# Kernel optimization log

Hardware: AMD Instinct MI355X
Metric: run time of the kernel (lower is better)

Reference implementation:

```python
import jax, jax.numpy as jnp
import numpy as np

N, E, P, D, G, L = 100000, 640000, 640000, 128, 128, 3
BN_EPS = 1e-5

def _bn(x, p):
    # eval-mode BatchNorm1d: p is stacked [gamma, beta, running_mean, running_var]
    g, b, m, v = p[0], p[1], p[2], p[3]
    return (x - m) * jax.lax.rsqrt(v + BN_EPS) * g + b

def setup_inputs() -> dict:
    key = jax.random.key(0)
    ks = iter(jax.random.split(key, 64))
    def nrm(shape, s):
        return jax.random.normal(next(ks), shape, jnp.float32) * s
    def bnp(shape):
        return jax.random.uniform(next(ks), shape, jnp.float32, 0.5, 1.5)
    inp = {}
    # graph data
    inp['x_node'] = jnp.zeros((N,), jnp.int32)
    inp['edge_index'] = jax.random.randint(next(ks), (2, E), 0, N, jnp.int32)
    inp['edge_attr'] = jax.random.normal(next(ks), (E, 7), jnp.float32)
    inp['batch'] = jnp.sort(jax.random.randint(next(ks), (N,), 0, G, jnp.int32))
    inp['pos_index'] = jax.random.randint(next(ks), (P,), 0, 1800, jnp.int32)
    inp['pos_enc'] = jax.random.uniform(next(ks), (P,), jnp.float32)
    inp['pos_batch'] = jnp.sort(jax.random.randint(next(ks), (P,), 0, E, jnp.int32))
    # encoders
    inp['node_emb'] = nrm((1, D), 1.0)                 # Embedding(1, D) for ogbg-ppa
    inp['z_init'] = nrm((1800, D), 1.0)                # z_initial embedding table
    inp['ze_bn1'] = bnp((4, D))
    inp['ze_W'] = nrm((D, D), D ** -0.5)
    inp['ze_b'] = jnp.zeros((D,), jnp.float32)
    inp['ze_bn2'] = bnp((4, D))
    inp['vn_emb'] = jnp.zeros((1, D), jnp.float32)     # init.constant_(0)
    # GINConv_eff per-layer params (stacked over L)
    inp['conv_We'] = nrm((L, 7, D), 7 ** -0.5)         # edge_encoder Linear(7, D)
    inp['conv_be'] = jnp.zeros((L, D), jnp.float32)
    inp['conv_Wp'] = nrm((L, D, D), D ** -0.5)         # edge_encoder_pos Linear(D, D)
    inp['conv_bp'] = jnp.zeros((L, D), jnp.float32)
    inp['conv_W1'] = nrm((L, D, 2 * D), D ** -0.5)     # mlp Linear(D, 2D)
    inp['conv_b1'] = jnp.zeros((L, 2 * D), jnp.float32)
    inp['conv_bn'] = bnp((L, 4, 2 * D))                # mlp BatchNorm(2D)
    inp['conv_W2'] = nrm((L, 2 * D, D), (2 * D) ** -0.5)  # mlp Linear(2D, D)
    inp['conv_b2'] = jnp.zeros((L, D), jnp.float32)
    inp['conv_eps'] = jnp.zeros((L,), jnp.float32)     # GIN eps, init 0
    inp['layer_bn'] = bnp((L, 4, D))                   # per-layer batch_norms
    # virtual-node MLPs (L-1 of them)
    inp['vn_W1'] = nrm((L - 1, D, 2 * D), D ** -0.5)
    inp['vn_b1'] = jnp.zeros((L - 1, 2 * D), jnp.float32)
    inp['vn_bn1'] = bnp((L - 1, 4, 2 * D))
    inp['vn_W2'] = nrm((L - 1, 2 * D, D), (2 * D) ** -0.5)
    inp['vn_b2'] = jnp.zeros((L - 1, D), jnp.float32)
    inp['vn_bn2'] = bnp((L - 1, 4, D))
    return inp

def reference(x_node, edge_index, edge_attr, batch, pos_index, pos_enc, pos_batch,
              node_emb, z_init, ze_bn1, ze_W, ze_b, ze_bn2, vn_emb,
              conv_We, conv_be, conv_Wp, conv_bp, conv_W1, conv_b1, conv_bn,
              conv_W2, conv_b2, conv_eps, layer_bn,
              vn_W1, vn_b1, vn_bn1, vn_W2, vn_b2, vn_bn2):
    src, dst = edge_index[0], edge_index[1]
    # node encoder (Embedding(1, D) indexed by zeros)
    h = node_emb[x_node]                                           # [N, D]
    # positional edge embedding: pool z_initial rows per edge, then z_embedding MLP
    z = jax.ops.segment_sum(z_init[pos_index] * pos_enc[:, None], pos_batch,
                            num_segments=E)                        # [E, D]
    z = jax.nn.relu(_bn(z, ze_bn1))
    z = jax.nn.relu(_bn(z @ ze_W + ze_b, ze_bn2))
    # virtual node embeddings, one per graph
    vn = jnp.broadcast_to(vn_emb[0], (G, D))
    for l in range(L):
        h_in = h + vn[batch]                                       # virtual-node broadcast add
        # GINConv_eff
        edge_emb = edge_attr @ conv_We[l] + conv_be[l] + z @ conv_Wp[l] + conv_bp[l]  # [E, D]
        msg = jax.nn.relu(h_in[src] + edge_emb)                    # gather + relu
        agg = jax.ops.segment_sum(msg, dst, num_segments=N)        # scatter-add
        t = (1.0 + conv_eps[l]) * h_in + agg
        t = jax.nn.relu(_bn(t @ conv_W1[l] + conv_b1[l], conv_bn[l]))
        out = t @ conv_W2[l] + conv_b2[l]
        out = _bn(out, layer_bn[l])                                # batch_norms[l]
        h = out if l == L - 1 else jax.nn.relu(out)                # dropout is identity (eval)
        if l < L - 1:
            vt = jax.ops.segment_sum(h_in, batch, num_segments=G) + vn
            vt = jax.nn.relu(_bn(vt @ vn_W1[l] + vn_b1[l], vn_bn1[l]))
            vn = jax.nn.relu(_bn(vt @ vn_W2[l] + vn_b2[l], vn_bn2[l]))
    return h  # JK == 'last'
```

## Files before the change

kernel.cpp:

```cpp
#include <hip/hip_runtime.h>
#include <hip/hip_bf16.h>

typedef __hip_bfloat16 bf16;
typedef __attribute__((ext_vector_type(8))) short short8;
typedef __attribute__((ext_vector_type(4))) float floatx4;

constexpr int Nn = 100000;
constexpr int Ee = 640000;
constexpr int Pp = 640000;
constexpr int Gg = 128;
constexpr int Ll = 3;
#define Dd 128
#define BN_EPS 1e-5f

__device__ __forceinline__ float b2f(bf16 x) { return __bfloat162float(x); }
__device__ __forceinline__ bf16 f2b(float x) { return __float2bfloat16(x); }
#define MFMA16 __builtin_amdgcn_mfma_f32_16x16x32_bf16

union U8 { uint4 u; bf16 h[8]; short8 s; };

__global__ void k_estart(const int* __restrict__ pos_batch, int* __restrict__ estart) {
  int e = blockIdx.x * blockDim.x + threadIdx.x;
  if (e > Ee) return;
  int lo = 0, hi = Pp;
  while (lo < hi) { int mid = (lo + hi) >> 1; if (pos_batch[mid] < e) lo = mid + 1; else hi = mid; }
  estart[e] = lo;
}

__global__ void k_hist(const int* __restrict__ dst, int* __restrict__ cnt) {
  int e = blockIdx.x * blockDim.x + threadIdx.x;
  if (e >= Ee) return;
  atomicAdd(&cnt[dst[e]], 1);
}

__global__ void k_scanA(const int* __restrict__ cnt, int* __restrict__ rs,
                        int* __restrict__ chunkSum) {
  __shared__ int buf[1024];
  int tid = threadIdx.x;
  int i = blockIdx.x * 1024 + tid;
  int v = (i < Nn) ? cnt[i] : 0;
  buf[tid] = v;
  __syncthreads();
  for (int off = 1; off < 1024; off <<= 1) {
    int t = (tid >= off) ? buf[tid - off] : 0;
    __syncthreads();
    buf[tid] += t;
    __syncthreads();
  }
  if (i < Nn) rs[i] = buf[tid] - v;
  if (tid == 1023) chunkSum[blockIdx.x] = buf[1023];
}

__global__ void k_scanC(int* __restrict__ rs, const int* __restrict__ chunkSum) {
  __shared__ int offS;
  if (threadIdx.x == 0) {
    int o = 0;
    for (int j = 0; j < blockIdx.x; ++j) o += chunkSum[j];
    offS = o;
  }
  __syncthreads();
  int i = blockIdx.x * 1024 + threadIdx.x;
  if (i < Nn) rs[i] += offS;
}

__global__ void k_scatter(const int* __restrict__ dst, const int* __restrict__ rs,
                          int* __restrict__ cur, int* __restrict__ perm) {
  int e = blockIdx.x * blockDim.x + threadIdx.x;
  if (e >= Ee) return;
  int d = dst[e];
  int r = atomicAdd(&cur[d], 1);
  perm[rs[d] + r] = e;
}

__global__ void k_permcopy(const int* __restrict__ perm, const int* __restrict__ src,
                           const int* __restrict__ dst, const int* __restrict__ estart,
                           const float* __restrict__ eattr,
                           int* __restrict__ src_p, int* __restrict__ dst_p,
                           int2* __restrict__ rng_p, bf16* __restrict__ ea_p) {
  int i = blockIdx.x * blockDim.x + threadIdx.x;
  if (i >= Ee) return;
  int e = perm[i];
  src_p[i] = src[e];
  dst_p[i] = dst[e];
  rng_p[i] = make_int2(estart[e], estart[e + 1]);
  U8 o;
  #pragma unroll
  for (int j = 0; j < 7; ++j) o.h[j] = f2b(eattr[(size_t)e * 7 + j]);
  o.h[7] = f2b(1.0f);
  ((uint4*)ea_p)[i] = o.u;
}

__global__ void k_prep(const float* __restrict__ zeW, const float* __restrict__ Wp,
                       const float* __restrict__ We, const float* __restrict__ be,
                       const float* __restrict__ bp,
                       const float* __restrict__ W1, const float* __restrict__ W2,
                       bf16* __restrict__ zeWsw, bf16* __restrict__ WpSw,
                       bf16* __restrict__ WeSw, bf16* __restrict__ W1sw,
                       bf16* __restrict__ W2sw) {
  int gid = blockIdx.x * blockDim.x + threadIdx.x;
  if (gid < 16384) {
    int i = gid;
    int j = i & 7, lane = (i >> 3) & 63, t = (i >> 9) & 7, kc = i >> 12;
    int k = kc * 32 + ((lane >> 4) * 8) + j, n = t * 16 + (lane & 15);
    zeWsw[i] = f2b(zeW[k * 128 + n]);
  }
  if (gid < 49152) {
    int l = gid / 16384, i = gid % 16384;
    int j = i & 7, lane = (i >> 3) & 63, t = (i >> 9) & 7, kc = i >> 12;
    int k = kc * 32 + ((lane >> 4) * 8) + j, n = t * 16 + (lane & 15);
    WpSw[gid] = f2b(Wp[l * 16384 + k * 128 + n]);
  }
  if (gid < 12288) {
    int l = gid / 4096, i = gid % 4096;
    int j = i & 7, lane = (i >> 3) & 63, t = i >> 9;
    int k = ((lane >> 4) * 8) + j, n = t * 16 + (lane & 15);
    float v = 0.f;
    if (k < 7) v = We[l * 896 + k * 128 + n];
    else if (k == 7) v = be[l * 128 + n] + bp[l * 128 + n];
    WeSw[gid] = f2b(v);
  }
  if (gid < 98304) {
    int l = gid / 32768, i = gid % 32768;
    int j = i & 7, lane = (i >> 3) & 63, t = (i >> 9) & 15, kc = i >> 13;
    int k = kc * 32 + ((lane >> 4) * 8) + j, n = t * 16 + (lane & 15);
    W1sw[gid] = f2b(W1[l * 32768 + k * 256 + n]);
  }
  if (gid < 98304) {
    int l = gid / 32768, i = gid % 32768;
    int j = i & 7, lane = (i >> 3) & 63, t = (i >> 9) & 7, kc = i >> 12;
    int k = kc * 32 + ((lane >> 4) * 8) + j, n = t * 16 + (lane & 15);
    W2sw[gid] = f2b(W2[l * 32768 + k * 128 + n]);
  }
}

__global__ void k_bnfold(const float* __restrict__ ze_bn1, const float* __restrict__ ze_b,
                         const float* __restrict__ ze_bn2,
                         const float* __restrict__ conv_b1, const float* __restrict__ conv_bn,
                         const float* __restrict__ conv_b2, const float* __restrict__ layer_bn,
                         const float* __restrict__ vn_b1, const float* __restrict__ vn_bn1,
                         const float* __restrict__ vn_b2, const float* __restrict__ vn_bn2,
                         float* __restrict__ fb) {
  int i = blockIdx.x * blockDim.x + threadIdx.x;
  if (i < 128) {
    float g = ze_bn1[i], b = ze_bn1[128 + i], m = ze_bn1[256 + i], v = ze_bn1[384 + i];
    float s = g * rsqrtf(v + BN_EPS);
    fb[i] = s; fb[128 + i] = b - m * s;
  } else if (i < 256) {
    int c = i - 128;
    float g = ze_bn2[c], b = ze_bn2[128 + c], m = ze_bn2[256 + c], v = ze_bn2[384 + c];
    float s = g * rsqrtf(v + BN_EPS);
    fb[256 + c] = s; fb[384 + c] = b - m * s + s * ze_b[c];
  } else if (i < 1024) {
    int j = i - 256; int l = j >> 8, c = j & 255;
    const float* bn = conv_bn + (size_t)l * 1024;
    float g = bn[c], b = bn[256 + c], m = bn[512 + c], v = bn[768 + c];
    float s = g * rsqrtf(v + BN_EPS);
    fb[512 + j] = s; fb[1280 + j] = b - m * s + s * conv_b1[l * 256 + c];
  } else if (i < 1408) {
    int j = i - 1024; int l = j >> 7, c = j & 127;
    const float* bn = layer_bn + (size_t)l * 512;
    float g = bn[c], b = bn[128 + c], m = bn[256 + c], v = bn[384 + c];
    float s = g * rsqrtf(v + BN_EPS);
    fb[2048 + j] = s; fb[2432 + j] = b - m * s + s * conv_b2[l * 128 + c];
  } else if (i < 1920) {
    int j = i - 1408; int l = j >> 8, c = j & 255;
    const float* bn = vn_bn1 + (size_t)l * 1024;
    float g = bn[c], b = bn[256 + c], m = bn[512 + c], v = bn[768 + c];
    float s = g * rsqrtf(v + BN_EPS);
    fb[2816 + j] = s; fb[3328 + j] = b - m * s + s * vn_b1[l * 256 + c];
  } else if (i < 2176) {
    int j = i - 1920; int l = j >> 7, c = j & 127;
    const float* bn = vn_bn2 + (size_t)l * 512;
    float g = bn[c], b = bn[128 + c], m = bn[256 + c], v = bn[384 + c];
    float s = g * rsqrtf(v + BN_EPS);
    fb[3840 + j] = s; fb[4096 + j] = b - m * s + s * vn_b2[l * 128 + c];
  }
}

__global__ void k_init_vn(const float* __restrict__ vn_emb, float* __restrict__ vn) {
  int gid = blockIdx.x * blockDim.x + threadIdx.x;
  if (gid >= Gg * 128) return;
  vn[gid] = vn_emb[gid & 127];
}

__global__ void k_hin0(const int* __restrict__ x_node, const float* __restrict__ node_emb,
                       const float* __restrict__ vn, const int* __restrict__ batch,
                       bf16* __restrict__ h_in) {
  int gid = blockIdx.x * blockDim.x + threadIdx.x;
  if (gid >= Nn * 16) return;
  int n = gid >> 4, c = gid & 15;
  int x = x_node[n], b = batch[n];
  float4 a0 = ((const float4*)node_emb)[x * 32 + c * 2];
  float4 a1 = ((const float4*)node_emb)[x * 32 + c * 2 + 1];
  float4 v0 = ((const float4*)vn)[b * 32 + c * 2];
  float4 v1 = ((const float4*)vn)[b * 32 + c * 2 + 1];
  U8 o;
  o.h[0] = f2b(a0.x + v0.x); o.h[1] = f2b(a0.y + v0.y);
  o.h[2] = f2b(a0.z + v0.z); o.h[3] = f2b(a0.w + v0.w);
  o.h[4] = f2b(a1.x + v1.x); o.h[5] = f2b(a1.y + v1.y);
  o.h[6] = f2b(a1.z + v1.z); o.h[7] = f2b(a1.w + v1.w);
  ((uint4*)h_in)[gid] = o.u;
}

__global__ __launch_bounds__(256, 4) void k_edge_z(
    const int2* __restrict__ rng_perm, const int* __restrict__ pos_index,
    const float* __restrict__ pos_enc, const float* __restrict__ z_init,
    const float* __restrict__ fb, const bf16* __restrict__ zeWsw,
    const bf16* __restrict__ ea_p, const int* __restrict__ src_p,
    const int* __restrict__ dst_p, const bf16* __restrict__ h_in,
    const bf16* __restrict__ WpSw, const bf16* __restrict__ WeSw,
    bf16* __restrict__ Z, int store_z, float* agg) {
  __shared__ bf16 Az[64][136];
  __shared__ int dstS[64];
  int tid = threadIdx.x;
  int lane = tid & 63, wv = tid >> 6;
  int q = lane >> 4, ln = lane & 15;
  int e0 = blockIdx.x * 64;

  if (q == 0) dstS[16 * wv + ln] = dst_p[e0 + 16 * wv + ln];
  short8 af0 = {};
  if (q == 0) af0 = *(const short8*)(ea_p + (size_t)(e0 + 16 * wv + ln) * 8);

  {
    int r = lane >> 2, cc = lane & 3;
    int2 rg = rng_perm[e0 + 16 * wv + r];
    float acc[32];
    #pragma unroll
    for (int j = 0; j < 32; ++j) acc[j] = 0.f;
    for (int p = rg.x; p < rg.y; ++p) {
      int idx = pos_index[p];
      float w = pos_enc[p];
      #pragma unroll
      for (int qq = 0; qq < 8; ++qq) {
        float4 z4 = ((const float4*)z_init)[idx * 32 + cc * 8 + qq];
        acc[qq * 4 + 0] = fmaf(w, z4.x, acc[qq * 4 + 0]);
        acc[qq * 4 + 1] = fmaf(w, z4.y, acc[qq * 4 + 1]);
        acc[qq * 4 + 2] = fmaf(w, z4.z, acc[qq * 4 + 2]);
        acc[qq * 4 + 3] = fmaf(w, z4.w, acc[qq * 4 + 3]);
      }
    }
    #pragma unroll
    for (int qq = 0; qq < 4; ++qq) {
      U8 o;
      #pragma unroll
      for (int jj = 0; jj < 2; ++jj) {
        int col = cc * 32 + qq * 8 + jj * 4;
        float4 s4 = *(const float4*)&fb[col];
        float4 h4 = *(const float4*)&fb[128 + col];
        o.h[jj * 4 + 0] = f2b(fmaxf(0.f, fmaf(acc[qq * 8 + jj * 4 + 0], s4.x, h4.x)));
        o.h[jj * 4 + 1] = f2b(fmaxf(0.f, fmaf(acc[qq * 8 + jj * 4 + 1], s4.y, h4.y)));
        o.h[jj * 4 + 2] = f2b(fmaxf(0.f, fmaf(acc[qq * 8 + jj * 4 + 2], s4.z, h4.z)));
        o.h[jj * 4 + 3] = f2b(fmaxf(0.f, fmaf(acc[qq * 8 + jj * 4 + 3], s4.w, h4.w)));
      }
      *(uint4*)&Az[16 * wv + r][cc * 32 + qq * 8] = o.u;
    }
  }
  __builtin_amdgcn_wave_barrier();

  {
    floatx4 acc1[8] = {};
    #pragma unroll
    for (int kc = 0; kc < 4; ++kc) {
      short8 af = *(const short8*)&Az[16 * wv + ln][kc * 32 + q * 8];
      #pragma unroll
      for (int t = 0; t < 8; ++t) {
        short8 bfr = *(const short8*)(zeWsw + (((size_t)kc * 8 + t) * 64 + lane) * 8);
        acc1[t] = MFMA16(af, bfr, acc1[t], 0, 0, 0);
      }
    }
    __builtin_amdgcn_wave_barrier();
    #pragma unroll
    for (int t = 0; t < 8; ++t) {
      int c = t * 16 + ln;
      float ss = fb[256 + c], hh = fb[384 + c];
      #pragma unroll
      for (int r = 0; r < 4; ++r)
        Az[16 * wv + q * 4 + r][c] = f2b(fmaxf(0.f, fmaf(acc1[t][r], ss, hh)));
    }
  }
  __builtin_amdgcn_wave_barrier();
  floatx4 acc2[8] = {};
  #pragma unroll
  for (int t = 0; t < 8; ++t) {
    short8 bfr = *(const short8*)(WeSw + ((size_t)t * 64 + lane) * 8);
    acc2[t] = MFMA16(af0, bfr, acc2[t], 0, 0, 0);
  }
  #pragma unroll
  for (int kc = 0; kc < 4; ++kc) {
    short8 af = *(const short8*)&Az[16 * wv + ln][kc * 32 + q * 8];
    #pragma unroll
    for (int t = 0; t < 8; ++t) {
      short8 bfr = *(const short8*)(WpSw + (((size_t)kc * 8 + t) * 64 + lane) * 8);
      acc2[t] = MFMA16(af, bfr, acc2[t], 0, 0, 0);
    }
  }
  __builtin_amdgcn_wave_barrier();
  if (store_z) {
    #pragma unroll
    for (int p = 0; p < 4; ++p) {
      int row = 16 * wv + p * 4 + q;
      uint4 vv = *(const uint4*)&Az[row][ln * 8];
      ((uint4*)Z)[(size_t)(e0 + row) * 16 + ln] = vv;
    }
  }
  __builtin_amdgcn_wave_barrier();
  #pragma unroll
  for (int p = 0; p < 4; ++p) {
    int el = 16 * wv + p * 4 + q;
    int s = src_p[e0 + el];
    uint4 hh = ((const uint4*)h_in)[(size_t)s * 16 + ln];
    *(uint4*)&Az[el][ln * 8] = hh;
  }
  __builtin_amdgcn_wave_barrier();
  #pragma unroll
  for (int t = 0; t < 8; ++t) {
    int c = t * 16 + ln;
    #pragma unroll
    for (int r = 0; r < 4; ++r) {
      int el = 16 * wv + q * 4 + r;
      Az[el][c] = f2b(fmaxf(0.f, acc2[t][r] + b2f(Az[el][c])));
    }
  }
  __builtin_amdgcn_wave_barrier();
  {
    float s0 = 0.f, s1 = 0.f;
    int dprev = dstS[16 * wv];
    bool inside = false;
    #pragma unroll
    for (int j = 0; j < 16; ++j) {
      int dcur = dstS[16 * wv + j];
      if (dcur != dprev) {
        float* ap = agg + (size_t)dprev * Dd;
        if (inside) { ap[lane] = s0; ap[64 + lane] = s1; }
        else        { atomicAdd(ap + lane, s0); atomicAdd(ap + 64 + lane, s1); }
        s0 = 0.f; s1 = 0.f; dprev = dcur; inside = true;
      }
      s0 += b2f(Az[16 * wv + j][lane]);
      s1 += b2f(Az[16 * wv + j][64 + lane]);
    }
    float* ap = agg + (size_t)dprev * Dd;
    atomicAdd(ap + lane, s0);
    atomicAdd(ap + 64 + lane, s1);
  }
}

__global__ __launch_bounds__(256, 6) void k_edge_fused(
    const bf16* __restrict__ Z, const bf16* __restrict__ ea_p,
    const int* __restrict__ src_p, const int* __restrict__ dst_p,
    const bf16* __restrict__ h_in,
    const bf16* __restrict__ WpSw, const bf16* __restrict__ WeSw,
    float* agg) {
  __shared__ bf16 Az[64][136];
  __shared__ int dstS[64];
  int tid = threadIdx.x;
  int lane = tid & 63, wv = tid >> 6;
  int q = lane >> 4, ln = lane & 15;
  int e0 = blockIdx.x * 64;

  if (q == 0) dstS[16 * wv + ln] = dst_p[e0 + 16 * wv + ln];

  short8 af0 = {};
  if (q == 0) af0 = *(const short8*)(ea_p + (size_t)(e0 + 16 * wv + ln) * 8);
  const bf16* zrow = Z + (size_t)(e0 + 16 * wv + ln) * 128 + q * 8;
  short8 zf0 = *(const short8*)(zrow);
  short8 zf1 = *(const short8*)(zrow + 32);
  short8 zf2 = *(const short8*)(zrow + 64);
  short8 zf3 = *(const short8*)(zrow + 96);

  #pragma unroll
  for (int p = 0; p < 4; ++p) {
    int el = 16 * wv + p * 4 + q;
    int s = src_p[e0 + el];
    uint4 hh = ((const uint4*)h_in)[(size_t)s * 16 + ln];
    *(uint4*)&Az[el][ln * 8] = hh;
  }
  __builtin_amdgcn_wave_barrier();

  #pragma unroll
  for (int tp = 0; tp < 4; ++tp) {
    const int t0 = tp * 2, t1 = tp * 2 + 1;
    floatx4 a0 = {}, a1 = {};
    a0 = MFMA16(af0, *(const short8*)(WeSw + ((size_t)t0 * 64 + lane) * 8), a0, 0, 0, 0);
    a1 = MFMA16(af0, *(const short8*)(WeSw + ((size_t)t1 * 64 + lane) * 8), a1, 0, 0, 0);
    a0 = MFMA16(zf0, *(const short8*)(WpSw + ((size_t)(t0) * 64 + lane) * 8), a0, 0, 0, 0);
    a1 = MFMA16(zf0, *(const short8*)(WpSw + ((size_t)(t1) * 64 + lane) * 8), a1, 0, 0, 0);
    a0 = MFMA16(zf1, *(const short8*)(WpSw + ((size_t)(8 + t0) * 64 + lane) * 8), a0, 0, 0, 0);
    a1 = MFMA16(zf1, *(const short8*)(WpSw + ((size_t)(8 + t1) * 64 + lane) * 8), a1, 0, 0, 0);
    a0 = MFMA16(zf2, *(const short8*)(WpSw + ((size_t)(16 + t0) * 64 + lane) * 8), a0, 0, 0, 0);
    a1 = MFMA16(zf2, *(const short8*)(WpSw + ((size_t)(16 + t1) * 64 + lane) * 8), a1, 0, 0, 0);
    a0 = MFMA16(zf3, *(const short8*)(WpSw + ((size_t)(24 + t0) * 64 + lane) * 8), a0, 0, 0, 0);
    a1 = MFMA16(zf3, *(const short8*)(WpSw + ((size_t)(24 + t1) * 64 + lane) * 8), a1, 0, 0, 0);
    int c0 = t0 * 16 + ln, c1 = t1 * 16 + ln;
    #pragma unroll
    for (int r = 0; r < 4; ++r) {
      int el = 16 * wv + q * 4 + r;
      Az[el][c0] = f2b(fmaxf(0.f, a0[r] + b2f(Az[el][c0])));
      Az[el][c1] = f2b(fmaxf(0.f, a1[r] + b2f(Az[el][c1])));
    }
  }
  __builtin_amdgcn_wave_barrier();
  {
    float s0 = 0.f, s1 = 0.f;
    int dprev = dstS[16 * wv];
    bool inside = false;
    #pragma unroll
    for (int j = 0; j < 16; ++j) {
      int dcur = dstS[16 * wv + j];
      if (dcur != dprev) {
        float* ap = agg + (size_t)dprev * Dd;
        if (inside) { ap[lane] = s0; ap[64 + lane] = s1; }
        else        { atomicAdd(ap + lane, s0); atomicAdd(ap + 64 + lane, s1); }
        s0 = 0.f; s1 = 0.f; dprev = dcur; inside = true;
      }
      s0 += b2f(Az[16 * wv + j][lane]);
      s1 += b2f(Az[16 * wv + j][64 + lane]);
    }
    float* ap = agg + (size_t)dprev * Dd;
    atomicAdd(ap + lane, s0);
    atomicAdd(ap + 64 + lane, s1);
  }
}

__global__ __launch_bounds__(256, 4) void k_mlp_fused(
    const bf16* __restrict__ h_in, float* agg,
    const float* __restrict__ eps_arr, int l,
    const int* __restrict__ batch, const float* __restrict__ vn,
    const bf16* __restrict__ W1sw, const float* __restrict__ Msc, const float* __restrict__ Msh,
    const bf16* __restrict__ W2sw, const float* __restrict__ Lsc, const float* __restrict__ Lsh,
    int is_last, int zero_agg, bf16* __restrict__ out_b, float* out_f) {
  __shared__ bf16 R[4][16][280];
  int tid = threadIdx.x;
  int lane = tid & 63, wv = tid >> 6;
  int q = lane >> 4, ln = lane & 15;
  int r0 = blockIdx.x * 64;
  float epsv = 1.0f + eps_arr[l];
  {
    int r = lane >> 2, cc = lane & 3;
    int row = r0 + 16 * wv + r;
    float4 z4 = make_float4(0.f, 0.f, 0.f, 0.f);
    #pragma unroll
    for (int u = 0; u < 4; ++u) {
      int cb = cc * 4 + u;
      U8 o;
      if (row < Nn) {
        U8 hh; hh.u = ((const uint4*)h_in)[row * 16 + cb];
        float4 g0 = ((const float4*)agg)[row * 32 + cb * 2];
        float4 g1 = ((const float4*)agg)[row * 32 + cb * 2 + 1];
        o.h[0] = f2b(epsv * b2f(hh.h[0]) + g0.x); o.h[1] = f2b(epsv * b2f(hh.h[1]) + g0.y);
        o.h[2] = f2b(epsv * b2f(hh.h[2]) + g0.z); o.h[3] = f2b(epsv * b2f(hh.h[3]) + g0.w);
        o.h[4] = f2b(epsv * b2f(hh.h[4]) + g1.x); o.h[5] = f2b(epsv * b2f(hh.h[5]) + g1.y);
        o.h[6] = f2b(epsv * b2f(hh.h[6]) + g1.z); o.h[7] = f2b(epsv * b2f(hh.h[7]) + g1.w);
        if (zero_agg) {
          ((float4*)agg)[row * 32 + cb * 2] = z4;
          ((float4*)agg)[row * 32 + cb * 2 + 1] = z4;
        }
      } else {
        o.u.x = o.u.y = o.u.z = o.u.w = 0;
      }
      *(uint4*)&R[wv][r][cb * 8] = o.u;
    }
  }
  __builtin_amdgcn_wave_barrier();
  {
    floatx4 acc1[8] = {};
    #pragma unroll
    for (int kc = 0; kc < 4; ++kc) {
      short8 af = *(const short8*)&R[wv][ln][kc * 32 + q * 8];
      #pragma unroll
      for (int t8 = 0; t8 < 8; ++t8) {
        int tt = 8 + t8;
        short8 bfr = *(const short8*)(W1sw + (size_t)l * 32768 + (((size_t)kc * 16 + tt) * 64 + lane) * 8);
        acc1[t8] = MFMA16(af, bfr, acc1[t8], 0, 0, 0);
      }
    }
    __builtin_amdgcn_wave_barrier();
    #pragma unroll
    for (int t8 = 0; t8 < 8; ++t8) {
      int c = (8 + t8) * 16 + ln;
      float ss = Msc[c], hh = Msh[c];
      #pragma unroll
      for (int r = 0; r < 4; ++r)
        R[wv][q * 4 + r][c] = f2b(fmaxf(0.f, fmaf(acc1[t8][r], ss, hh)));
    }
  }
  {
    floatx4 acc1[8] = {};
    #pragma unroll
    for (int kc = 0; kc < 4; ++kc) {
      short8 af = *(const short8*)&R[wv][ln][kc * 32 + q * 8];
      #pragma unroll
      for (int t8 = 0; t8 < 8; ++t8) {
        short8 bfr = *(const short8*)(W1sw + (size_t)l * 32768 + (((size_t)kc * 16 + t8) * 64 + lane) * 8);
        acc1[t8] = MFMA16(af, bfr, acc1[t8], 0, 0, 0);
      }
    }
    __builtin_amdgcn_wave_barrier();
    #pragma unroll
    for (int t8 = 0; t8 < 8; ++t8) {
      int c = t8 * 16 + ln;
      float ss = Msc[c], hh = Msh[c];
      #pragma unroll
      for (int r = 0; r < 4; ++r)
        R[wv][q * 4 + r][c] = f2b(fmaxf(0.f, fmaf(acc1[t8][r], ss, hh)));
    }
  }
  __builtin_amdgcn_wave_barrier();
  int bb[4] = {0, 0, 0, 0};
  if (!is_last) {
    #pragma unroll
    for (int r = 0; r < 4; ++r) {
      int row = r0 + 16 * wv + q * 4 + r;
      if (row < Nn) bb[r] = batch[row];
    }
  }
  #pragma unroll
  for (int g2 = 0; g2 < 2; ++g2) {
    floatx4 acc2[4] = {};
    #pragma unroll
    for (int kc = 0; kc < 8; ++kc) {
      short8 af = *(const short8*)&R[wv][ln][kc * 32 + q * 8];
      #pragma unroll
      for (int t4 = 0; t4 < 4; ++t4) {
        int tt = g2 * 4 + t4;
        short8 bfr = *(const short8*)(W2sw + (size_t)l * 32768 + (((size_t)kc * 8 + tt) * 64 + lane) * 8);
        acc2[t4] = MFMA16(af, bfr, acc2[t4], 0, 0, 0);
      }
    }
    #pragma unroll
    for (int t4 = 0; t4 < 4; ++t4) {
      int tt = g2 * 4 + t4;
      int c = tt * 16 + ln;
      float ss = Lsc[c], hh = Lsh[c];
      #pragma unroll
      for (int r = 0; r < 4; ++r) {
        int row = r0 + 16 * wv + q * 4 + r;
        if (row < Nn) {
          float x = fmaf(acc2[t4][r], ss, hh);
          if (is_last) out_f[(size_t)row * Dd + c] = x;
          else         out_b[(size_t)row * Dd + c] = f2b(fmaxf(0.f, x) + vn[bb[r] * Dd + c]);
        }
      }
    }
  }
}

__global__ void k_vt_sum(const bf16* __restrict__ h_in, const int* __restrict__ batch,
                         float* __restrict__ vt) {
  int d = threadIdx.x;
  int chunk = (Nn + gridDim.x - 1) / gridDim.x;
  int r0 = blockIdx.x * chunk;
  int r1 = min(r0 + chunk, Nn);
  if (r0 >= r1) return;
  float acc = 0.f;
  int cur = batch[r0];
  for (int r = r0; r < r1; ++r) {
    int g = batch[r];
    if (g != cur) { atomicAdd(&vt[cur * Dd + d], acc); acc = 0.f; cur = g; }
    acc += b2f(h_in[r * Dd + d]);
  }
  atomicAdd(&vt[cur * Dd + d], acc);
}

__global__ __launch_bounds__(256) void k_vn_mlp(
    float* __restrict__ vn, const float* __restrict__ vt,
    const float* __restrict__ W1, const float* __restrict__ s1, const float* __restrict__ h1,
    const float* __restrict__ W2, const float* __restrict__ s2, const float* __restrict__ h2) {
  __shared__ float row[128];
  __shared__ float trow[256];
  int g = blockIdx.x;
  int tid = threadIdx.x;
  if (tid < 128) row[tid] = vt[g * Dd + tid] + vn[g * Dd + tid];
  __syncthreads();
  float acc = 0.f;
  for (int k = 0; k < 128; ++k) acc += row[k] * W1[k * 256 + tid];
  trow[tid] = fmaxf(0.f, fmaf(acc, s1[tid], h1[tid]));
  __syncthreads();
  if (tid < 128) {
    float acc2 = 0.f;
    for (int k = 0; k < 256; ++k) acc2 += trow[k] * W2[k * Dd + tid];
    vn[g * Dd + tid] = fmaxf(0.f, fmaf(acc2, s2[tid], h2[tid]));
  }
}

extern "C" void kernel_launch(void* const* d_in, const int* in_sizes, int n_in,
                              void* d_out, int out_size, void* d_ws, size_t ws_size,
                              hipStream_t stream) {
  const int*   x_node    = (const int*)  d_in[0];
  const int*   edge_idx  = (const int*)  d_in[1];
  const float* edge_attr = (const float*)d_in[2];
  const int*   batch     = (const int*)  d_in[3];
  const int*   pos_index = (const int*)  d_in[4];
  const float* pos_enc   = (const float*)d_in[5];
  const int*   pos_batch = (const int*)  d_in[6];
  const float* node_emb  = (const float*)d_in[7];
  const float* z_init    = (const float*)d_in[8];
  const float* ze_bn1    = (const float*)d_in[9];
  const float* ze_W      = (const float*)d_in[10];
  const float* ze_b      = (const float*)d_in[11];
  const float* ze_bn2    = (const float*)d_in[12];
  const float* vn_emb    = (const float*)d_in[13];
  const float* conv_We   = (const float*)d_in[14];
  const float* conv_be   = (const float*)d_in[15];
  const float* conv_Wp   = (const float*)d_in[16];
  const float* conv_bp   = (const float*)d_in[17];
  const float* conv_W1   = (const float*)d_in[18];
  const float* conv_b1   = (const float*)d_in[19];
  const float* conv_bn   = (const float*)d_in[20];
  const float* conv_W2   = (const float*)d_in[21];
  const float* conv_b2   = (const float*)d_in[22];
  const float* conv_eps  = (const float*)d_in[23];
  const float* layer_bn  = (const float*)d_in[24];
  const float* vn_W1     = (const float*)d_in[25];
  const float* vn_b1     = (const float*)d_in[26];
  const float* vn_bn1    = (const float*)d_in[27];
  const float* vn_W2     = (const float*)d_in[28];
  const float* vn_b2     = (const float*)d_in[29];
  const float* vn_bn2    = (const float*)d_in[30];

  char* wb = (char*)d_ws;
  size_t o = 0;
  auto alloc = [&](size_t bytes) { void* p = wb + o; o += (bytes + 255) & ~255ull; return p; };
  bf16*  h_in     = (bf16*) alloc((size_t)Nn * 128 * 2);
  float* vn       = (float*)alloc((size_t)Gg * 128 * 4);
  float* vt       = (float*)alloc((size_t)Gg * 128 * 4);
  int*   estart   = (int*)  alloc((size_t)(Ee + 1) * 4);
  bf16*  zeWsw    = (bf16*) alloc(16384 * 2);
  bf16*  WpSw     = (bf16*) alloc(49152 * 2);
  bf16*  WeSw     = (bf16*) alloc(12288 * 2);
  bf16*  W1sw     = (bf16*) alloc(98304 * 2);
  bf16*  W2sw     = (bf16*) alloc(98304 * 2);
  float* fb       = (float*)alloc(4352 * 4);
  int*   cnt      = (int*)  alloc((size_t)Nn * 4);
  int*   rs       = (int*)  alloc((size_t)Nn * 4);
  int*   cur      = (int*)  alloc((size_t)Nn * 4);
  int*   chunkSum = (int*)  alloc(128 * 4);
  int*   perm     = (int*)  alloc((size_t)Ee * 4);
  int*   src_p    = (int*)  alloc((size_t)Ee * 4);
  int*   dst_p    = (int*)  alloc((size_t)Ee * 4);
  int2*  rng_p    = (int2*) alloc((size_t)Ee * 8);
  bf16*  ea_p     = (bf16*) alloc((size_t)Ee * 8 * 2);
  bf16*  Z        = (bf16*) alloc((size_t)Ee * 128 * 2);
  float* agg      = (float*)d_out;
  bool useZ = (o <= ws_size);

  const int* src = edge_idx;
  const int* dst = edge_idx + Ee;

  k_estart<<<(Ee + 256) / 256, 256, 0, stream>>>(pos_batch, estart);
  hipMemsetAsync(cnt, 0, (size_t)Nn * 4, stream);
  hipMemsetAsync(cur, 0, (size_t)Nn * 4, stream);
  k_hist<<<(Ee + 255) / 256, 256, 0, stream>>>(dst, cnt);
  int nchunk = (Nn + 1023) / 1024;
  k_scanA<<<nchunk, 1024, 0, stream>>>(cnt, rs, chunkSum);
  k_scanC<<<nchunk, 1024, 0, stream>>>(rs, chunkSum);
  k_scatter<<<(Ee + 255) / 256, 256, 0, stream>>>(dst, rs, cur, perm);
  k_permcopy<<<(Ee + 255) / 256, 256, 0, stream>>>(perm, src, dst, estart, edge_attr,
                                                   src_p, dst_p, rng_p, ea_p);
  k_prep<<<(98304 + 255) / 256, 256, 0, stream>>>(ze_W, conv_Wp, conv_We, conv_be, conv_bp,
                                                  conv_W1, conv_W2,
                                                  zeWsw, WpSw, WeSw, W1sw, W2sw);
  k_bnfold<<<9, 256, 0, stream>>>(ze_bn1, ze_b, ze_bn2, conv_b1, conv_bn,
                                  conv_b2, layer_bn, vn_b1, vn_bn1, vn_b2, vn_bn2, fb);
  k_init_vn<<<(Gg * 128 + 255) / 256, 256, 0, stream>>>(vn_emb, vn);
  k_hin0<<<(Nn * 16 + 255) / 256, 256, 0, stream>>>(x_node, node_emb, vn, batch, h_in);
  hipMemsetAsync(agg, 0, (size_t)Nn * 128 * 4, stream);

  int mblocks = (Nn + 63) / 64;
  for (int l = 0; l < Ll; ++l) {
    if (l == 0 || !useZ)
      k_edge_z<<<Ee / 64, 256, 0, stream>>>(rng_p, pos_index, pos_enc, z_init,
          fb, zeWsw, ea_p, src_p, dst_p, h_in,
          WpSw + (size_t)l * 16384, WeSw + (size_t)l * 4096,
          Z, (l == 0 && useZ) ? 1 : 0, agg);
    else
      k_edge_fused<<<Ee / 64, 256, 0, stream>>>(Z, ea_p, src_p, dst_p, h_in,
          WpSw + (size_t)l * 16384, WeSw + (size_t)l * 4096, agg);
    if (l < Ll - 1) {
      hipMemsetAsync(vt, 0, (size_t)Gg * 128 * 4, stream);
      k_vt_sum<<<1024, 128, 0, stream>>>(h_in, batch, vt);
      k_vn_mlp<<<Gg, 256, 0, stream>>>(vn, vt,
          vn_W1 + (size_t)l * 128 * 256, fb + 2816 + l * 256, fb + 3328 + l * 256,
          vn_W2 + (size_t)l * 256 * 128, fb + 3840 + l * 128, fb + 4096 + l * 128);
    }
    k_mlp_fused<<<mblocks, 256, 0, stream>>>(h_in, agg, conv_eps, l, batch, vn,
        W1sw, fb + 512 + l * 256, fb + 1280 + l * 256,
        W2sw, fb + 2048 + l * 128, fb + 2432 + l * 128,
        (l == Ll - 1) ? 1 : 0, (l < Ll - 1) ? 1 : 0, h_in, (float*)d_out);
  }
}
```

Measured before the change: 1.082 ms.

## Cut register pressure in edge kernels and raise launch-bound occupancy

The positional-encoding gather in k_edge_z now uses 8 lanes per row with 16 accumulators over two sequential passes, instead of 4 lanes per row with 32 accumulators. The edge-attribute fragment load is moved down next to its MFMA use so it is not live across the gather. Both edge kernels get launch bounds of 8 blocks per CU, aiming for more resident waves to hide gather latency. The cost is two serial passes over variable-length position ranges and a possible register spill under the tighter register budget.

```diff
diff --git a/kernel.cpp b/kernel.cpp
--- a/kernel.cpp
+++ b/kernel.cpp
@@ -202,7 +202,7 @@
   ((uint4*)h_in)[gid] = o.u;
 }
 
-__global__ __launch_bounds__(256, 4) void k_edge_z(
+__global__ __launch_bounds__(256, 8) void k_edge_z(
     const int2* __restrict__ rng_perm, const int* __restrict__ pos_index,
     const float* __restrict__ pos_enc, const float* __restrict__ z_init,
     const float* __restrict__ fb, const bf16* __restrict__ zeWsw,
@@ -218,41 +218,43 @@
   int e0 = blockIdx.x * 64;
 
   if (q == 0) dstS[16 * wv + ln] = dst_p[e0 + 16 * wv + ln];
-  short8 af0 = {};
-  if (q == 0) af0 = *(const short8*)(ea_p + (size_t)(e0 + 16 * wv + ln) * 8);
-
-  {
-    int r = lane >> 2, cc = lane & 3;
-    int2 rg = rng_perm[e0 + 16 * wv + r];
-    float acc[32];
-    #pragma unroll
-    for (int j = 0; j < 32; ++j) acc[j] = 0.f;
-    for (int p = rg.x; p < rg.y; ++p) {
-      int idx = pos_index[p];
-      float w = pos_enc[p];
-      #pragma unroll
-      for (int qq = 0; qq < 8; ++qq) {
-        float4 z4 = ((const float4*)z_init)[idx * 32 + cc * 8 + qq];
-        acc[qq * 4 + 0] = fmaf(w, z4.x, acc[qq * 4 + 0]);
-        acc[qq * 4 + 1] = fmaf(w, z4.y, acc[qq * 4 + 1]);
-        acc[qq * 4 + 2] = fmaf(w, z4.z, acc[qq * 4 + 2]);
-        acc[qq * 4 + 3] = fmaf(w, z4.w, acc[qq * 4 + 3]);
-      }
-    }
-    #pragma unroll
-    for (int qq = 0; qq < 4; ++qq) {
-      U8 o;
-      #pragma unroll
-      for (int jj = 0; jj < 2; ++jj) {
-        int col = cc * 32 + qq * 8 + jj * 4;
-        float4 s4 = *(const float4*)&fb[col];
-        float4 h4 = *(const float4*)&fb[128 + col];
-        o.h[jj * 4 + 0] = f2b(fmaxf(0.f, fmaf(acc[qq * 8 + jj * 4 + 0], s4.x, h4.x)));
-        o.h[jj * 4 + 1] = f2b(fmaxf(0.f, fmaf(acc[qq * 8 + jj * 4 + 1], s4.y, h4.y)));
-        o.h[jj * 4 + 2] = f2b(fmaxf(0.f, fmaf(acc[qq * 8 + jj * 4 + 2], s4.z, h4.z)));
-        o.h[jj * 4 + 3] = f2b(fmaxf(0.f, fmaf(acc[qq * 8 + jj * 4 + 3], s4.w, h4.w)));
-      }
-      *(uint4*)&Az[16 * wv + r][cc * 32 + qq * 8] = o.u;
+
+  {
+    int r = lane >> 3, cc = lane & 7;
+    #pragma unroll 1
+    for (int pass = 0; pass < 2; ++pass) {
+      int row = 16 * wv + pass * 8 + r;
+      int2 rg = rng_perm[e0 + row];
+      float acc[16];
+      #pragma unroll
+      for (int j = 0; j < 16; ++j) acc[j] = 0.f;
+      for (int p = rg.x; p < rg.y; ++p) {
+        int idx = pos_index[p];
+        float w = pos_enc[p];
+        #pragma unroll
+        for (int u = 0; u < 4; ++u) {
+          float4 z4 = ((const float4*)z_init)[idx * 32 + cc * 4 + u];
+          acc[u * 4 + 0] = fmaf(w, z4.x, acc[u * 4 + 0]);
+          acc[u * 4 + 1] = fmaf(w, z4.y, acc[u * 4 + 1]);
+          acc[u * 4 + 2] = fmaf(w, z4.z, acc[u * 4 + 2]);
+          acc[u * 4 + 3] = fmaf(w, z4.w, acc[u * 4 + 3]);
+        }
+      }
+      #pragma unroll
+      for (int u2 = 0; u2 < 2; ++u2) {
+        U8 o;
+        #pragma unroll
+        for (int jj = 0; jj < 2; ++jj) {
+          int col = cc * 16 + u2 * 8 + jj * 4;
+          float4 s4 = *(const float4*)&fb[col];
+          float4 h4 = *(const float4*)&fb[128 + col];
+          o.h[jj * 4 + 0] = f2b(fmaxf(0.f, fmaf(acc[u2 * 8 + jj * 4 + 0], s4.x, h4.x)));
+          o.h[jj * 4 + 1] = f2b(fmaxf(0.f, fmaf(acc[u2 * 8 + jj * 4 + 1], s4.y, h4.y)));
+          o.h[jj * 4 + 2] = f2b(fmaxf(0.f, fmaf(acc[u2 * 8 + jj * 4 + 2], s4.z, h4.z)));
+          o.h[jj * 4 + 3] = f2b(fmaxf(0.f, fmaf(acc[u2 * 8 + jj * 4 + 3], s4.w, h4.w)));
+        }
+        *(uint4*)&Az[row][cc * 16 + u2 * 8] = o.u;
+      }
     }
   }
   __builtin_amdgcn_wave_barrier();
@@ -280,10 +282,14 @@
   }
   __builtin_amdgcn_wave_barrier();
   floatx4 acc2[8] = {};
-  #pragma unroll
-  for (int t = 0; t < 8; ++t) {
-    short8 bfr = *(const short8*)(WeSw + ((size_t)t * 64 + lane) * 8);
-    acc2[t] = MFMA16(af0, bfr, acc2[t], 0, 0, 0);
+  {
+    short8 af0 = {};
+    if (q == 0) af0 = *(const short8*)(ea_p + (size_t)(e0 + 16 * wv + ln) * 8);
+    #pragma unroll
+    for (int t = 0; t < 8; ++t) {
+      short8 bfr = *(const short8*)(WeSw + ((size_t)t * 64 + lane) * 8);
+      acc2[t] = MFMA16(af0, bfr, acc2[t], 0, 0, 0);
+    }
   }
   #pragma unroll
   for (int kc = 0; kc < 4; ++kc) {
@@ -344,7 +350,7 @@
   }
 }
 
-__global__ __launch_bounds__(256, 6) void k_edge_fused(
+__global__ __launch_bounds__(256, 8) void k_edge_fused(
     const bf16* __restrict__ Z, const bf16* __restrict__ ea_p,
     const int* __restrict__ src_p, const int* __restrict__ dst_p,
     const bf16* __restrict__ h_in,
```

New measurement: 1.147 ms. 6.0% more time.
